# Performance work log

Hardware: AMD Instinct MI355X
Metric: run time of the kernel (lower is better)

The kernel has to match this reference:

```python
import jax, jax.numpy as jnp
from jax import lax
import numpy as np

DATA_DIM, DATA_NUM, CTX_DIM, PB_DIM, HID_DIM, T = 6, 30, 180, 2, 240, 8192


def setup_inputs() -> dict:
    key = jax.random.key(0)
    ks = jax.random.split(key, 12)
    f = lambda k, s: jax.random.normal(k, s, dtype=jnp.float32)
    return {
        "data": f(ks[0], (DATA_NUM, DATA_DIM, T)),
        "W1d": f(ks[1], (HID_DIM, DATA_DIM)) * 0.1,
        "b1d": f(ks[2], (HID_DIM,)) * 0.1,
        "W1p": f(ks[3], (HID_DIM, PB_DIM)) * 0.1,
        "b1p": f(ks[4], (HID_DIM,)) * 0.1,
        "W1c": f(ks[5], (HID_DIM, CTX_DIM)) * 0.05,
        "b1c": f(ks[6], (HID_DIM,)) * 0.1,
        "W2d": f(ks[7], (DATA_DIM, HID_DIM)) * 0.1,
        "b2d": f(ks[8], (DATA_DIM,)) * 0.1,
        "W2c": f(ks[9], (CTX_DIM, HID_DIM)) * 0.05,
        "b2c": f(ks[10], (CTX_DIM,)) * 0.1,
        "pb": f(ks[11], (DATA_NUM, PB_DIM)) * 0.1,
    }


def reference(data, W1d, b1d, W1p, b1p, W1c, b1c, W2d, b2d, W2c, b2c, pb):
    # Teacher-forcing path (GENERATE=False): each timestep's input is data[:, :, t];
    # only ctx is carried through the recurrence.
    # Precompute the time-varying + pb input projections for all steps: [T, B, H]
    pre = (jnp.einsum('bdt,hd->tbh', data, W1d) + b1d
           + (pb @ W1p.T + b1p)[None, :, :])

    def step(ctx, pre_t):
        h = jax.nn.relu(pre_t + ctx @ W1c.T + b1c)   # [B, H]
        out = h @ W2d.T + b2d                        # [B, data_dim]
        new_ctx = h @ W2c.T + b2c                    # [B, ctx_dim]
        return new_ctx, out

    ctx0 = jnp.zeros((data.shape[0], CTX_DIM), dtype=data.dtype)
    _, outs = lax.scan(step, ctx0, pre)              # outs: [T, B, data_dim]
    return jnp.transpose(outs, (1, 0, 2))            # [B, T, data_dim] (stack dim=1)
```

## Files before the change

### kernel.cpp

```cpp
#include <hip/hip_runtime.h>
#include <hip/hip_bf16.h>
#include <stdint.h>


#define T_STEPS 8192
#define HID     240
#define CTX     180
#define KTOT    256
#define HXROW   264
#define HXBUF   (16*HXROW)
#define A_HALVES (256*256)
#define SCRATCH_BYTES (A_HALVES*2 + 16)

typedef __hip_bfloat16 bf16;
typedef _Float16 f16;
typedef _Float16 half8  __attribute__((ext_vector_type(8)));
typedef _Float16 half4v __attribute__((ext_vector_type(4)));
typedef float    f32x4  __attribute__((ext_vector_type(4)));
typedef float    f32x2  __attribute__((ext_vector_type(2)));

#define MFMA16(A,B,C) __builtin_amdgcn_mfma_f32_16x16x32_f16((A),(B),(C),0,0,0)

__device__ __forceinline__ float ldin(const void* p, long i, bool f32) {
    return f32 ? ((const float*)p)[i] : __bfloat162float(((const bf16*)p)[i]);
}
__device__ __forceinline__ unsigned pkbf(float a, float b) {
    unsigned ua = (unsigned)__builtin_bit_cast(unsigned short, __float2bfloat16(a));
    unsigned ub = (unsigned)__builtin_bit_cast(unsigned short, __float2bfloat16(b));
    return ua | (ub << 16);
}
__device__ __forceinline__ void barrier_lds() {
    asm volatile("s_waitcnt lgkmcnt(0)\n\ts_barrier" ::: "memory");
}

__global__ __launch_bounds__(64) void detect_dtype(const void* data, int* flag) {
    unsigned int w  = ((const unsigned int*)data)[threadIdx.x];
    unsigned int lo = w & 0xFFFFu;
    unsigned int ex = (lo >> 7) & 0xFFu;
    unsigned long long huge = __ballot(ex >= 0x8Eu);
    unsigned long long zero = __ballot(lo == 0u);
    if (threadIdx.x == 0) *flag = (huge != 0ull || zero == ~0ull) ? 1 : 0;
}

__global__ __launch_bounds__(256) void build_A(
    const void* __restrict__ W1d, const void* __restrict__ b1d,
    const void* __restrict__ W1p, const void* __restrict__ b1p,
    const void* __restrict__ W1c, const void* __restrict__ b1c,
    const void* __restrict__ W2d, const void* __restrict__ b2d,
    const void* __restrict__ W2c, const void* __restrict__ b2c,
    f16* __restrict__ Aa, const int* __restrict__ flagp)
{
    const bool f32 = (*flagp != 0);
    int idx = blockIdx.x*256 + threadIdx.x;
    int r = idx >> 8, k = idx & 255;
    float v = 0.f;
    if (r < HID) {
        if (k < HID) {
            float acc = 0.f;
            for (int c = 0; c < CTX; ++c)
                acc = fmaf(ldin(W1c, r*CTX+c, f32), ldin(W2c, c*HID+k, f32), acc);
            v = acc;
        } else if (k < 246) {
            v = ldin(W1d, r*6 + (k-240), f32);
        } else if (k == 246) {
            float m0 = 0.f;
            for (int c = 0; c < CTX; ++c)
                m0 = fmaf(ldin(W1c, r*CTX+c, f32), ldin(b2c, c, f32), m0);
            v = ldin(b1d, r, f32) + ldin(b1c, r, f32) + ldin(b1p, r, f32) + m0;
        } else if (k <= 248) {
            v = ldin(W1p, r*2 + (k-247), f32);
        }
    } else if (r < 246) {
        int o = r - 240;
        if (k < HID)       v = ldin(W2d, o*HID + k, f32);
        else if (k == 246) v = ldin(b2d, o, f32);
    }
    Aa[idx] = (f16)v;
}

__global__ __launch_bounds__(512, 2) void rnn_mfma(
    const void* __restrict__ data,
    const void* __restrict__ b1d, const void* __restrict__ W1p,
    const void* __restrict__ b1p, const void* __restrict__ b1c,
    const void* __restrict__ W1d, const void* __restrict__ pb,
    const f16* __restrict__ Aa, const int* __restrict__ flagp,
    void* __restrict__ out)
{
    const bool f32 = (*flagp != 0);
    const int tid  = threadIdx.x;
    const int w    = tid >> 6;
    const int l    = tid & 63;
    const int n16  = l & 15;
    const int quad = l >> 4;
    const int base = blockIdx.x * 16;
    const int bn   = base + n16;
    const bool bvalid = (bn < 30);

    __shared__ __align__(16) f16 Hx[2*HXBUF];

    {
        int* hz = (int*)Hx;
        for (int i = tid; i < HXBUF; i += 512) hz[i] = 0;
    }
    __syncthreads();

    if (tid < 32) {
        int bsel = tid >> 4, n = tid & 15;
        int nb = base + n; if (nb > 29) nb = 29;
        f16* col = Hx + bsel*HXBUF + n*HXROW;
        col[246] = (f16)1.0f;
        col[247] = (f16)ldin(pb, nb*2+0, f32);
        col[248] = (f16)ldin(pb, nb*2+1, f32);
    }

    for (int p = tid; p < HID*16; p += 512) {
        int n = p / HID, j = p - n*HID;
        int nb = base + n; if (nb > 29) nb = 29;
        float s = ldin(b1d, j, f32) + ldin(b1c, j, f32) + ldin(b1p, j, f32)
                + ldin(W1p, j*2+0, f32)*ldin(pb, nb*2+0, f32)
                + ldin(W1p, j*2+1, f32)*ldin(pb, nb*2+1, f32);
        for (int d = 0; d < 6; ++d)
            s = fmaf(ldin(W1d, j*6+d, f32), ldin(data, ((long)nb*6+d)*T_STEPS, f32), s);
        Hx[n*HXROW + j] = (f16)fmaxf(s, 0.f);
    }

    const int pn = tid & 15, pd = tid >> 4;
    int pnb = base + pn; if (pnb > 29) pnb = 29;
    const long prow = ((long)pnb*6 + (pd < 6 ? pd : 0))*T_STEPS;

    if (tid < 96)
        Hx[pn*HXROW + 240 + pd] = (f16)ldin(data, prow + 1, f32);

    unsigned u0 = 0, u1 = 0;
    if (tid < 96) {
        if (!f32) {
            u0 = ((const unsigned short*)data)[prow + 2];
            u1 = ((const unsigned short*)data)[prow + 3];
        } else {
            u0 = __builtin_bit_cast(unsigned, ((const float*)data)[prow + 2]);
            u1 = __builtin_bit_cast(unsigned, ((const float*)data)[prow + 3]);
        }
    }

    const f16* Ab0 = Aa + (size_t)((w*2+0)*16 + n16)*KTOT + quad*8;
    const f16* Ab1 = Aa + (size_t)((w*2+1)*16 + n16)*KTOT + quad*8;
    half8 a00 = *(const half8*)(Ab0 +   0), a01 = *(const half8*)(Ab0 +  32);
    half8 a02 = *(const half8*)(Ab0 +  64), a03 = *(const half8*)(Ab0 +  96);
    half8 a04 = *(const half8*)(Ab0 + 128), a05 = *(const half8*)(Ab0 + 160);
    half8 a06 = *(const half8*)(Ab0 + 192), a07 = *(const half8*)(Ab0 + 224);
    half8 a10 = *(const half8*)(Ab1 +   0), a11 = *(const half8*)(Ab1 +  32);
    half8 a12 = *(const half8*)(Ab1 +  64), a13 = *(const half8*)(Ab1 +  96);
    half8 a14 = *(const half8*)(Ab1 + 128), a15 = *(const half8*)(Ab1 + 160);
    half8 a16 = *(const half8*)(Ab1 + 192), a17 = *(const half8*)(Ab1 + 224);
    asm volatile("s_waitcnt vmcnt(0)" ::: "memory");
    __syncthreads();

    const f16* hxread0 = Hx + n16*HXROW + quad*8;
    f16*       hxw     = Hx + n16*HXROW + quad*4;

    for (int t2 = 0; t2 < T_STEPS; t2 += 2) {
        #pragma unroll
        for (int s = 0; s < 2; ++s) {
            const int t = t2 + s;
            const int cur = s, nxt = s ^ 1;

            if (tid < 96) {
                unsigned uc = (s == 0) ? u0 : u1;
                float dv = f32 ? __builtin_bit_cast(float, uc)
                               : __builtin_bit_cast(float, uc << 16);
                Hx[nxt*HXBUF + pn*HXROW + 240 + pd] = (f16)dv;
                long g = t + 4; if (g > T_STEPS-1) g = T_STEPS-1;
                unsigned un;
                if (!f32) un = ((const unsigned short*)data)[prow + g];
                else      un = __builtin_bit_cast(unsigned, ((const float*)data)[prow + g]);
                if (s == 0) u0 = un; else u1 = un;
            }

            const f16* hxc = hxread0 + cur*HXBUF;
            half8 b0 = *(const half8*)(hxc +   0);
            half8 b1 = *(const half8*)(hxc +  32);
            half8 b2 = *(const half8*)(hxc +  64);
            f32x4 c0 = {0.f,0.f,0.f,0.f}, c1 = {0.f,0.f,0.f,0.f};
            half8 b3 = *(const half8*)(hxc +  96);
            c0 = MFMA16(a00, b0, c0);  c1 = MFMA16(a10, b0, c1);
            half8 b4 = *(const half8*)(hxc + 128);
            c0 = MFMA16(a01, b1, c0);  c1 = MFMA16(a11, b1, c1);
            half8 b5 = *(const half8*)(hxc + 160);
            c0 = MFMA16(a02, b2, c0);  c1 = MFMA16(a12, b2, c1);
            half8 b6 = *(const half8*)(hxc + 192);
            c0 = MFMA16(a03, b3, c0);  c1 = MFMA16(a13, b3, c1);
            half8 b7 = *(const half8*)(hxc + 224);
            c0 = MFMA16(a04, b4, c0);  c1 = MFMA16(a14, b4, c1);
            c0 = MFMA16(a05, b5, c0);  c1 = MFMA16(a15, b5, c1);
            c0 = MFMA16(a06, b6, c0);  c1 = MFMA16(a16, b6, c1);
            c0 = MFMA16(a07, b7, c0);  c1 = MFMA16(a17, b7, c1);

            f16* hxn = hxw + nxt*HXBUF;
            {
                half4v hv;
                hv.x = (f16)fmaxf(c0.x, 0.f);
                hv.y = (f16)fmaxf(c0.y, 0.f);
                hv.z = (f16)fmaxf(c0.z, 0.f);
                hv.w = (f16)fmaxf(c0.w, 0.f);
                *(half4v*)(hxn + (2*w)*16) = hv;
            }
            if (w < 7) {
                half4v hv;
                hv.x = (f16)fmaxf(c1.x, 0.f);
                hv.y = (f16)fmaxf(c1.y, 0.f);
                hv.z = (f16)fmaxf(c1.z, 0.f);
                hv.w = (f16)fmaxf(c1.w, 0.f);
                *(half4v*)(hxn + (2*w+1)*16) = hv;
            } else if (bvalid) {
                long ob = ((long)bn*T_STEPS + t)*6;
                if (quad == 0) {
                    if (!f32) {
                        bf16* op = (bf16*)out + ob;
                        *(unsigned*)(op)     = pkbf(c1.x, c1.y);
                        *(unsigned*)(op + 2) = pkbf(c1.z, c1.w);
                    } else {
                        float* op = (float*)out + ob;
                        f32x2 p0 = {c1.x, c1.y}; *(f32x2*)(op)     = p0;
                        f32x2 p1 = {c1.z, c1.w}; *(f32x2*)(op + 2) = p1;
                    }
                } else if (quad == 1) {
                    if (!f32) {
                        bf16* op = (bf16*)out + ob;
                        *(unsigned*)(op + 4) = pkbf(c1.x, c1.y);
                    } else {
                        float* op = (float*)out + ob;
                        f32x2 p0 = {c1.x, c1.y}; *(f32x2*)(op + 4) = p0;
                    }
                }
            }
            barrier_lds();
        }
    }
}

extern "C" void kernel_launch(void* const* d_in, const int* in_sizes, int n_in,
                              void* d_out, int out_size, void* d_ws, size_t ws_size,
                              hipStream_t stream) {
    const void* data = d_in[0];
    const void* W1d  = d_in[1];
    const void* b1d  = d_in[2];
    const void* W1p  = d_in[3];
    const void* b1p  = d_in[4];
    const void* W1c  = d_in[5];
    const void* b1c  = d_in[6];
    const void* W2d  = d_in[7];
    const void* b2d  = d_in[8];
    const void* W2c  = d_in[9];
    const void* b2c  = d_in[10];
    const void* pb   = d_in[11];

    size_t need = SCRATCH_BYTES;
    char* scratch;
    if (ws_size >= need) {
        scratch = (char*)d_ws;
    } else {
        size_t out_bytes = (size_t)30*T_STEPS*6*sizeof(bf16);
        scratch = (char*)d_out + ((out_bytes - need) & ~(size_t)255);
    }
    f16* Aa    = (f16*)scratch;
    int* flagp = (int*)(scratch + A_HALVES*2);

    detect_dtype<<<1, 64, 0, stream>>>(data, flagp);
    build_A<<<A_HALVES/256, 256, 0, stream>>>(W1d, b1d, W1p, b1p, W1c, b1c,
                                              W2d, b2d, W2c, b2c, Aa, flagp);
    rnn_mfma<<<2, 512, 0, stream>>>(data, b1d, W1p, b1p, b1c, W1d, pb,
                                    Aa, flagp, d_out);
}
```

Before: 3.927 ms.

## Use four waves per block with four MFMA tiles each instead of eight

Reduces the recurrent kernel's block from 512 to 256 threads, with each wave now owning four 16-row tiles of the fused weight matrix held in registers instead of two. Fewer waves participate in the per-step LDS barrier, cutting synchronisation overhead in the latency-bound 8192-step loop. The cost is more register pressure per wave and twice as many MFMAs issued serially per wave each step.

```diff
diff --git a/kernel.cpp b/kernel.cpp
--- a/kernel.cpp
+++ b/kernel.cpp
@@ -78,7 +78,7 @@
     Aa[idx] = (f16)v;
 }
 
-__global__ __launch_bounds__(512, 2) void rnn_mfma(
+__global__ __launch_bounds__(256, 1) void rnn_mfma(
     const void* __restrict__ data,
     const void* __restrict__ b1d, const void* __restrict__ W1p,
     const void* __restrict__ b1p, const void* __restrict__ b1c,
@@ -100,7 +100,7 @@
 
     {
         int* hz = (int*)Hx;
-        for (int i = tid; i < HXBUF; i += 512) hz[i] = 0;
+        for (int i = tid; i < HXBUF; i += 256) hz[i] = 0;
     }
     __syncthreads();
 
@@ -113,7 +113,7 @@
         col[248] = (f16)ldin(pb, nb*2+1, f32);
     }
 
-    for (int p = tid; p < HID*16; p += 512) {
+    for (int p = tid; p < HID*16; p += 256) {
         int n = p / HID, j = p - n*HID;
         int nb = base + n; if (nb > 29) nb = 29;
         float s = ldin(b1d, j, f32) + ldin(b1c, j, f32) + ldin(b1p, j, f32)
@@ -142,16 +142,26 @@
         }
     }
 
-    const f16* Ab0 = Aa + (size_t)((w*2+0)*16 + n16)*KTOT + quad*8;
-    const f16* Ab1 = Aa + (size_t)((w*2+1)*16 + n16)*KTOT + quad*8;
-    half8 a00 = *(const half8*)(Ab0 +   0), a01 = *(const half8*)(Ab0 +  32);
-    half8 a02 = *(const half8*)(Ab0 +  64), a03 = *(const half8*)(Ab0 +  96);
-    half8 a04 = *(const half8*)(Ab0 + 128), a05 = *(const half8*)(Ab0 + 160);
-    half8 a06 = *(const half8*)(Ab0 + 192), a07 = *(const half8*)(Ab0 + 224);
-    half8 a10 = *(const half8*)(Ab1 +   0), a11 = *(const half8*)(Ab1 +  32);
-    half8 a12 = *(const half8*)(Ab1 +  64), a13 = *(const half8*)(Ab1 +  96);
-    half8 a14 = *(const half8*)(Ab1 + 128), a15 = *(const half8*)(Ab1 + 160);
-    half8 a16 = *(const half8*)(Ab1 + 192), a17 = *(const half8*)(Ab1 + 224);
+    const f16* Ab0 = Aa + (size_t)((w*4+0)*16 + n16)*KTOT + quad*8;
+    const f16* Ab1 = Aa + (size_t)((w*4+1)*16 + n16)*KTOT + quad*8;
+    const f16* Ab2 = Aa + (size_t)((w*4+2)*16 + n16)*KTOT + quad*8;
+    const f16* Ab3 = Aa + (size_t)((w*4+3)*16 + n16)*KTOT + quad*8;
+    half8 A00 = *(const half8*)(Ab0 +   0), A01 = *(const half8*)(Ab0 +  32);
+    half8 A02 = *(const half8*)(Ab0 +  64), A03 = *(const half8*)(Ab0 +  96);
+    half8 A04 = *(const half8*)(Ab0 + 128), A05 = *(const half8*)(Ab0 + 160);
+    half8 A06 = *(const half8*)(Ab0 + 192), A07 = *(const half8*)(Ab0 + 224);
+    half8 A10 = *(const half8*)(Ab1 +   0), A11 = *(const half8*)(Ab1 +  32);
+    half8 A12 = *(const half8*)(Ab1 +  64), A13 = *(const half8*)(Ab1 +  96);
+    half8 A14 = *(const half8*)(Ab1 + 128), A15 = *(const half8*)(Ab1 + 160);
+    half8 A16 = *(const half8*)(Ab1 + 192), A17 = *(const half8*)(Ab1 + 224);
+    half8 A20 = *(const half8*)(Ab2 +   0), A21 = *(const half8*)(Ab2 +  32);
+    half8 A22 = *(const half8*)(Ab2 +  64), A23 = *(const half8*)(Ab2 +  96);
+    half8 A24 = *(const half8*)(Ab2 + 128), A25 = *(const half8*)(Ab2 + 160);
+    half8 A26 = *(const half8*)(Ab2 + 192), A27 = *(const half8*)(Ab2 + 224);
+    half8 A30 = *(const half8*)(Ab3 +   0), A31 = *(const half8*)(Ab3 +  32);
+    half8 A32 = *(const half8*)(Ab3 +  64), A33 = *(const half8*)(Ab3 +  96);
+    half8 A34 = *(const half8*)(Ab3 + 128), A35 = *(const half8*)(Ab3 + 160);
+    half8 A36 = *(const half8*)(Ab3 + 192), A37 = *(const half8*)(Ab3 + 224);
     asm volatile("s_waitcnt vmcnt(0)" ::: "memory");
     __syncthreads();
 
@@ -181,19 +191,28 @@
             half8 b1 = *(const half8*)(hxc +  32);
             half8 b2 = *(const half8*)(hxc +  64);
             f32x4 c0 = {0.f,0.f,0.f,0.f}, c1 = {0.f,0.f,0.f,0.f};
+            f32x4 c2 = {0.f,0.f,0.f,0.f}, c3 = {0.f,0.f,0.f,0.f};
             half8 b3 = *(const half8*)(hxc +  96);
-            c0 = MFMA16(a00, b0, c0);  c1 = MFMA16(a10, b0, c1);
+            c0 = MFMA16(A00, b0, c0);  c1 = MFMA16(A10, b0, c1);
+            c2 = MFMA16(A20, b0, c2);  c3 = MFMA16(A30, b0, c3);
             half8 b4 = *(const half8*)(hxc + 128);
-            c0 = MFMA16(a01, b1, c0);  c1 = MFMA16(a11, b1, c1);
+            c0 = MFMA16(A01, b1, c0);  c1 = MFMA16(A11, b1, c1);
+            c2 = MFMA16(A21, b1, c2);  c3 = MFMA16(A31, b1, c3);
             half8 b5 = *(const half8*)(hxc + 160);
-            c0 = MFMA16(a02, b2, c0);  c1 = MFMA16(a12, b2, c1);
+            c0 = MFMA16(A02, b2, c0);  c1 = MFMA16(A12, b2, c1);
+            c2 = MFMA16(A22, b2, c2);  c3 = MFMA16(A32, b2, c3);
             half8 b6 = *(const half8*)(hxc + 192);
-            c0 = MFMA16(a03, b3, c0);  c1 = MFMA16(a13, b3, c1);
+            c0 = MFMA16(A03, b3, c0);  c1 = MFMA16(A13, b3, c1);
+            c2 = MFMA16(A23, b3, c2);  c3 = MFMA16(A33, b3, c3);
             half8 b7 = *(const half8*)(hxc + 224);
-            c0 = MFMA16(a04, b4, c0);  c1 = MFMA16(a14, b4, c1);
-            c0 = MFMA16(a05, b5, c0);  c1 = MFMA16(a15, b5, c1);
-            c0 = MFMA16(a06, b6, c0);  c1 = MFMA16(a16, b6, c1);
-            c0 = MFMA16(a07, b7, c0);  c1 = MFMA16(a17, b7, c1);
+            c0 = MFMA16(A04, b4, c0);  c1 = MFMA16(A14, b4, c1);
+            c2 = MFMA16(A24, b4, c2);  c3 = MFMA16(A34, b4, c3);
+            c0 = MFMA16(A05, b5, c0);  c1 = MFMA16(A15, b5, c1);
+            c2 = MFMA16(A25, b5, c2);  c3 = MFMA16(A35, b5, c3);
+            c0 = MFMA16(A06, b6, c0);  c1 = MFMA16(A16, b6, c1);
+            c2 = MFMA16(A26, b6, c2);  c3 = MFMA16(A36, b6, c3);
+            c0 = MFMA16(A07, b7, c0);  c1 = MFMA16(A17, b7, c1);
+            c2 = MFMA16(A27, b7, c2);  c3 = MFMA16(A37, b7, c3);
 
             f16* hxn = hxw + nxt*HXBUF;
             {
@@ -202,34 +221,50 @@
                 hv.y = (f16)fmaxf(c0.y, 0.f);
                 hv.z = (f16)fmaxf(c0.z, 0.f);
                 hv.w = (f16)fmaxf(c0.w, 0.f);
-                *(half4v*)(hxn + (2*w)*16) = hv;
-            }
-            if (w < 7) {
+                *(half4v*)(hxn + (4*w+0)*16) = hv;
+            }
+            {
                 half4v hv;
                 hv.x = (f16)fmaxf(c1.x, 0.f);
                 hv.y = (f16)fmaxf(c1.y, 0.f);
                 hv.z = (f16)fmaxf(c1.z, 0.f);
                 hv.w = (f16)fmaxf(c1.w, 0.f);
-                *(half4v*)(hxn + (2*w+1)*16) = hv;
+                *(half4v*)(hxn + (4*w+1)*16) = hv;
+            }
+            {
+                half4v hv;
+                hv.x = (f16)fmaxf(c2.x, 0.f);
+                hv.y = (f16)fmaxf(c2.y, 0.f);
+                hv.z = (f16)fmaxf(c2.z, 0.f);
+                hv.w = (f16)fmaxf(c2.w, 0.f);
+                *(half4v*)(hxn + (4*w+2)*16) = hv;
+            }
+            if (w < 3) {
+                half4v hv;
+                hv.x = (f16)fmaxf(c3.x, 0.f);
+                hv.y = (f16)fmaxf(c3.y, 0.f);
+                hv.z = (f16)fmaxf(c3.z, 0.f);
+                hv.w = (f16)fmaxf(c3.w, 0.f);
+                *(half4v*)(hxn + (4*w+3)*16) = hv;
             } else if (bvalid) {
                 long ob = ((long)bn*T_STEPS + t)*6;
                 if (quad == 0) {
                     if (!f32) {
                         bf16* op = (bf16*)out + ob;
-                        *(unsigned*)(op)     = pkbf(c1.x, c1.y);
-                        *(unsigned*)(op + 2) = pkbf(c1.z, c1.w);
+                        *(unsigned*)(op)     = pkbf(c3.x, c3.y);
+                        *(unsigned*)(op + 2) = pkbf(c3.z, c3.w);
                     } else {
                         float* op = (float*)out + ob;
-                        f32x2 p0 = {c1.x, c1.y}; *(f32x2*)(op)     = p0;
-                        f32x2 p1 = {c1.z, c1.w}; *(f32x2*)(op + 2) = p1;
+                        f32x2 p0 = {c3.x, c3.y}; *(f32x2*)(op)     = p0;
+                        f32x2 p1 = {c3.z, c3.w}; *(f32x2*)(op + 2) = p1;
                     }
                 } else if (quad == 1) {
                     if (!f32) {
                         bf16* op = (bf16*)out + ob;
-                        *(unsigned*)(op + 4) = pkbf(c1.x, c1.y);
+                        *(unsigned*)(op + 4) = pkbf(c3.x, c3.y);
                     } else {
                         float* op = (float*)out + ob;
-                        f32x2 p0 = {c1.x, c1.y}; *(f32x2*)(op + 4) = p0;
+                        f32x2 p0 = {c3.x, c3.y}; *(f32x2*)(op + 4) = p0;
                     }
                 }
             }
@@ -268,6 +303,6 @@
     detect_dtype<<<1, 64, 0, stream>>>(data, flagp);
     build_A<<<A_HALVES/256, 256, 0, stream>>>(W1d, b1d, W1p, b1p, W1c, b1c,
                                               W2d, b2d, W2c, b2c, Aa, flagp);
-    rnn_mfma<<<2, 512, 0, stream>>>(data, b1d, W1p, b1p, b1c, W1d, pb,
+    rnn_mfma<<<2, 256, 0, stream>>>(data, b1d, W1p, b1p, b1c, W1d, pb,
                                     Aa, flagp, d_out);
 }
```

Result: slower. 4.287 ms (+9.2%).
